# Performance work log

Hardware: AMD Instinct MI355X
Metric: run time of the kernel (lower is better)

The kernel has to match this reference:

```python
import jax, jax.numpy as jnp
import numpy as np

B, Q, D = 8, 1, 4096
NH, NKV, HD = 32, 8, 128
KV = 4096
ROPE_BASE = 10000.0


def setup_inputs() -> dict:
    key = jax.random.key(0)
    ks = jax.random.split(key, 10)
    s = 0.02  # realistic init scale for weights
    return {
        "hidden_states": jax.random.normal(ks[0], (B, Q, D), jnp.float32),
        "past_k": jax.random.normal(ks[1], (B, NH, KV, HD), jnp.float32),
        "past_v": jax.random.normal(ks[2], (B, NH, KV, HD), jnp.float32),
        "Wq": jax.random.normal(ks[3], (NH * HD, D), jnp.float32) * s,
        "bq": jax.random.normal(ks[4], (NH * HD,), jnp.float32) * s,
        "Wk": jax.random.normal(ks[5], (NKV * HD, D), jnp.float32) * s,
        "bk": jax.random.normal(ks[6], (NKV * HD,), jnp.float32) * s,
        "Wv": jax.random.normal(ks[7], (NKV * HD, D), jnp.float32) * s,
        "bv": jax.random.normal(ks[8], (NKV * HD,), jnp.float32) * s,
        "Wo": jax.random.normal(ks[9], (D, NH * HD), jnp.float32) * s,
        "position_ids": KV,  # current decode position (past length)
    }


def _rope(x, pos0):
    # x: [B, H, Q, HD]; rotate_half-style RoPE at positions pos0..pos0+Q-1
    half = HD // 2
    inv_freq = 1.0 / (ROPE_BASE ** (jnp.arange(half, dtype=jnp.float32) / half))
    pos = (pos0 + jnp.arange(Q)).astype(jnp.float32)          # [Q]
    ang = pos[:, None] * inv_freq[None, :]                    # [Q, half]
    cos = jnp.concatenate([jnp.cos(ang), jnp.cos(ang)], -1)   # [Q, HD]
    sin = jnp.concatenate([jnp.sin(ang), jnp.sin(ang)], -1)
    x1, x2 = x[..., :half], x[..., half:]
    rot = jnp.concatenate([-x2, x1], axis=-1)
    return x * cos + rot * sin


def reference(hidden_states, past_k, past_v, Wq, bq, Wk, bk, Wv, bv, Wo, position_ids):
    # QKV projections (Qwen: biased q/k/v, unbiased o)
    q = hidden_states @ Wq.T + bq   # [B, Q, NH*HD]
    k = hidden_states @ Wk.T + bk   # [B, Q, NKV*HD]
    v = hidden_states @ Wv.T + bv
    q = q.reshape(B, Q, NH, HD).transpose(0, 2, 1, 3)    # [B, NH, Q, HD]
    k = k.reshape(B, Q, NKV, HD).transpose(0, 2, 1, 3)   # [B, NKV, Q, HD]
    v = v.reshape(B, Q, NKV, HD).transpose(0, 2, 1, 3)
    # RoPE on current tokens only (past cache already rotated)
    q = _rope(q, position_ids)
    k = _rope(k, position_ids)
    # GQA repeat_interleave to full head count
    rep = NH // NKV
    k = jnp.repeat(k, rep, axis=1)   # [B, NH, Q, HD]
    v = jnp.repeat(v, rep, axis=1)
    # Assemble streaming KV window: past cache is stored post-repeat
    k = jnp.concatenate([past_k, k], axis=2)   # [B, NH, KV+Q, HD]
    v = jnp.concatenate([past_v, v], axis=2)
    scale = jnp.float32(1.0 / np.sqrt(HD))
    scores = jnp.einsum("bhqd,bhkd->bhqk", q, k) * scale   # [B, NH, Q, KV+Q]
    # causal: query positions KV..KV+Q-1 attend to key positions <= own pos
    qpos = KV + jnp.arange(Q)
    kpos = jnp.arange(KV + Q)
    mask = qpos[:, None] >= kpos[None, :]
    scores = jnp.where(mask, scores, jnp.float32(-1e30))
    attn = jax.nn.softmax(scores, axis=-1)
    ctx = jnp.einsum("bhqk,bhkd->bhqd", attn, v)           # [B, NH, Q, HD]
    ctx = ctx.transpose(0, 2, 1, 3).reshape(B, Q, NH * HD)
    return ctx @ Wo.T   # [B, Q, D]
```

## Files before the change

kernel.cpp:

```cpp
#include <hip/hip_runtime.h>
#include <hip/hip_bf16.h>
#include <math.h>

#define BB 8
#define DD 4096
#define NHQ 32
#define NKV 8
#define HD 128
#define KVL 4096
#define NSPLIT 32
#define CHUNK (KVL / NSPLIT)
#define SCALE 0.08838834764831845f

#define OFF_QROPE 0
#define OFF_KROPE (OFF_QROPE + BB*NHQ*HD)
#define OFF_VRAW  (OFF_KROPE + BB*NKV*HD)
#define OFF_PART  (OFF_VRAW  + BB*NKV*HD)
#define PART_STRIDE 132
#define OFF_CTX   (OFF_PART + BB*NHQ*NSPLIT*PART_STRIDE)

typedef float f32x4 __attribute__((ext_vector_type(4)));

__device__ __forceinline__ float4 ntload4(const float4* p) {
    f32x4 v = __builtin_nontemporal_load((const f32x4*)p);
    return make_float4(v.x, v.y, v.z, v.w);
}

__global__ __launch_bounds__(256) void k_qkv(
    const float* __restrict__ hs,
    const float* __restrict__ Wq, const float* __restrict__ bq,
    const float* __restrict__ Wk, const float* __restrict__ bk,
    const float* __restrict__ Wv, const float* __restrict__ bv,
    const int* __restrict__ posp,
    float* __restrict__ ws)
{
    const int wid  = threadIdx.x >> 6;
    const int lane = threadIdx.x & 63;
    const int w    = blockIdx.x * 4 + wid;

    const float* W; const float* bias; float* dst; int dstride; int r1; int i; bool rope;
    if (w < 2048) {
        const int h = w >> 6; i = w & 63; r1 = h*HD + i;
        W = Wq; bias = bq; dst = ws + OFF_QROPE; dstride = NHQ*HD; rope = true;
    } else if (w < 2560) {
        const int w2 = w - 2048; const int h = w2 >> 6; i = w2 & 63; r1 = h*HD + i;
        W = Wk; bias = bk; dst = ws + OFF_KROPE; dstride = NKV*HD; rope = true;
    } else {
        const int w3 = w - 2560; const int h = w3 >> 6; i = w3 & 63; r1 = h*HD + i;
        W = Wv; bias = bv; dst = ws + OFF_VRAW; dstride = NKV*HD; rope = false;
    }
    const int r2 = r1 + 64;

    const double pos = (double)posp[0];
    const double ang = pos * pow(10000.0, -(double)i / 64.0);
    const float c = (float)cos(ang), s = (float)sin(ang);

    const float4* WrA = (const float4*)(W + (size_t)r1 * DD);
    const float4* WrB = (const float4*)(W + (size_t)r2 * DD);
    const float4* H   = (const float4*)hs;

    float accA[BB], accB[BB];
    #pragma unroll
    for (int b = 0; b < BB; ++b) { accA[b] = 0.f; accB[b] = 0.f; }

    for (int it = 0; it < DD/256; ++it) {
        const int idx = it*64 + lane;
        const float4 wa = ntload4(&WrA[idx]);
        const float4 wb = ntload4(&WrB[idx]);
        #pragma unroll
        for (int b = 0; b < BB; ++b) {
            const float4 h4 = H[b*(DD/4) + idx];
            accA[b] = fmaf(wa.x, h4.x, fmaf(wa.y, h4.y, fmaf(wa.z, h4.z, fmaf(wa.w, h4.w, accA[b]))));
            accB[b] = fmaf(wb.x, h4.x, fmaf(wb.y, h4.y, fmaf(wb.z, h4.z, fmaf(wb.w, h4.w, accB[b]))));
        }
    }
    #pragma unroll
    for (int b = 0; b < BB; ++b) {
        float va = accA[b], vb = accB[b];
        #pragma unroll
        for (int off = 32; off; off >>= 1) {
            va += __shfl_xor(va, off, 64);
            vb += __shfl_xor(vb, off, 64);
        }
        accA[b] = va; accB[b] = vb;
    }
    if (lane == 0) {
        const float b1 = bias[r1], b2 = bias[r2];
        #pragma unroll
        for (int b = 0; b < BB; ++b) {
            const float a1 = accA[b] + b1;
            const float a2 = accB[b] + b2;
            float o1, o2;
            if (rope) { o1 = fmaf(a1, c, -a2*s); o2 = fmaf(a2, c, a1*s); }
            else      { o1 = a1;                 o2 = a2; }
            dst[(size_t)b*dstride + r1] = o1;
            dst[(size_t)b*dstride + r2] = o2;
        }
    }
}

__global__ __launch_bounds__(256) void k_attn(
    const float* __restrict__ Kc, const float* __restrict__ Vc,
    float* __restrict__ ws)
{
    const int wid  = threadIdx.x >> 6;
    const int lane = threadIdx.x & 63;
    const int sub  = lane >> 5, l32 = lane & 31;
    const int task  = blockIdx.x * 4 + wid;
    const int pair  = task >> 5;
    const int split = task & (NSPLIT - 1);
    const int b = pair >> 5, h = pair & 31;

    const float4 q4 = ((const float4*)(ws + OFF_QROPE + (size_t)pair * HD))[l32];
    const size_t base = ((size_t)pair * KVL + (size_t)split * CHUNK) * HD;
    const float4* Kp = (const float4*)(Kc + base);
    const float4* Vp = (const float4*)(Vc + base);

    float m = -1e30f, l = 0.f;
    float4 acc = {0.f, 0.f, 0.f, 0.f};

    for (int it = 0; it < CHUNK/8; ++it) {
        const int r0 = it*8 + sub;
        const float4 k0 = ntload4(&Kp[(r0+0)*32 + l32]);
        const float4 k1 = ntload4(&Kp[(r0+2)*32 + l32]);
        const float4 k2 = ntload4(&Kp[(r0+4)*32 + l32]);
        const float4 k3 = ntload4(&Kp[(r0+6)*32 + l32]);
        const float4 v0 = ntload4(&Vp[(r0+0)*32 + l32]);
        const float4 v1 = ntload4(&Vp[(r0+2)*32 + l32]);
        const float4 v2 = ntload4(&Vp[(r0+4)*32 + l32]);
        const float4 v3 = ntload4(&Vp[(r0+6)*32 + l32]);

        float s0 = fmaf(q4.x, k0.x, fmaf(q4.y, k0.y, fmaf(q4.z, k0.z, q4.w*k0.w)));
        float s1 = fmaf(q4.x, k1.x, fmaf(q4.y, k1.y, fmaf(q4.z, k1.z, q4.w*k1.w)));
        float s2 = fmaf(q4.x, k2.x, fmaf(q4.y, k2.y, fmaf(q4.z, k2.z, q4.w*k2.w)));
        float s3 = fmaf(q4.x, k3.x, fmaf(q4.y, k3.y, fmaf(q4.z, k3.z, q4.w*k3.w)));
        #pragma unroll
        for (int off = 16; off; off >>= 1) {
            s0 += __shfl_xor(s0, off, 64);
            s1 += __shfl_xor(s1, off, 64);
            s2 += __shfl_xor(s2, off, 64);
            s3 += __shfl_xor(s3, off, 64);
        }
        s0 *= SCALE; s1 *= SCALE; s2 *= SCALE; s3 *= SCALE;

        const float newm = fmaxf(fmaxf(fmaxf(s0, s1), fmaxf(s2, s3)), m);
        const float r_ = __expf(m - newm);
        const float e0 = __expf(s0 - newm);
        const float e1 = __expf(s1 - newm);
        const float e2 = __expf(s2 - newm);
        const float e3 = __expf(s3 - newm);
        m = newm;
        l = fmaf(l, r_, (e0 + e1) + (e2 + e3));
        acc.x = fmaf(acc.x, r_, fmaf(e0, v0.x, e1*v1.x) + fmaf(e2, v2.x, e3*v3.x));
        acc.y = fmaf(acc.y, r_, fmaf(e0, v0.y, e1*v1.y) + fmaf(e2, v2.y, e3*v3.y));
        acc.z = fmaf(acc.z, r_, fmaf(e0, v0.z, e1*v1.z) + fmaf(e2, v2.z, e3*v3.z));
        acc.w = fmaf(acc.w, r_, fmaf(e0, v0.w, e1*v1.w) + fmaf(e2, v2.w, e3*v3.w));
    }

    if (split == NSPLIT - 1 && sub == 0) {
        const float4 k4 = ((const float4*)(ws + OFF_KROPE + (size_t)(b*NKV + (h>>2)) * HD))[l32];
        const float4 v4 = ((const float4*)(ws + OFF_VRAW  + (size_t)(b*NKV + (h>>2)) * HD))[l32];
        float sv = fmaf(q4.x, k4.x, fmaf(q4.y, k4.y, fmaf(q4.z, k4.z, q4.w*k4.w)));
        #pragma unroll
        for (int off = 16; off; off >>= 1) sv += __shfl_xor(sv, off, 64);
        sv *= SCALE;
        const float newm = fmaxf(m, sv);
        const float r_ = __expf(m - newm);
        const float e  = __expf(sv - newm);
        m = newm;
        l = fmaf(l, r_, e);
        acc.x = fmaf(acc.x, r_, e*v4.x);
        acc.y = fmaf(acc.y, r_, e*v4.y);
        acc.z = fmaf(acc.z, r_, e*v4.z);
        acc.w = fmaf(acc.w, r_, e*v4.w);
    }

    const float M  = fmaxf(m, __shfl_xor(m, 32, 64));
    const float r_ = __expf(m - M);
    l *= r_; acc.x *= r_; acc.y *= r_; acc.z *= r_; acc.w *= r_;
    l     += __shfl_xor(l,     32, 64);
    acc.x += __shfl_xor(acc.x, 32, 64);
    acc.y += __shfl_xor(acc.y, 32, 64);
    acc.z += __shfl_xor(acc.z, 32, 64);
    acc.w += __shfl_xor(acc.w, 32, 64);

    if (sub == 0) {
        float* pp = ws + OFF_PART + ((size_t)pair * NSPLIT + split) * PART_STRIDE;
        ((float4*)pp)[l32] = acc;
        if (l32 == 0) { pp[HD] = M; pp[HD+1] = l; }
    }
}

__global__ __launch_bounds__(128) void k_combine(float* __restrict__ ws)
{
    const int pair = blockIdx.x;
    const int d = threadIdx.x;
    const float* pp = ws + OFF_PART + (size_t)pair * NSPLIT * PART_STRIDE;
    __shared__ float sm[NSPLIT], sl[NSPLIT];
    if (d < NSPLIT) { sm[d] = pp[d*PART_STRIDE + HD]; sl[d] = pp[d*PART_STRIDE + HD + 1]; }
    __syncthreads();
    float M = -1e30f;
    #pragma unroll
    for (int s = 0; s < NSPLIT; ++s) M = fmaxf(M, sm[s]);
    float L = 0.f, acc = 0.f;
    #pragma unroll 8
    for (int s = 0; s < NSPLIT; ++s) {
        const float w = expf(sm[s] - M);
        L += sl[s] * w;
        acc = fmaf(pp[s*PART_STRIDE + d], w, acc);
    }
    ws[OFF_CTX + (size_t)pair*HD + d] = acc / L;
}

__global__ __launch_bounds__(256) void k_oproj(
    const float* __restrict__ Wo, const float* __restrict__ ws, float* __restrict__ out)
{
    const int wid  = threadIdx.x >> 6;
    const int lane = threadIdx.x & 63;
    const int row  = blockIdx.x * 4 + wid;
    const float4* Wr = (const float4*)(Wo + (size_t)row * DD);
    const float4* C  = (const float4*)(ws + OFF_CTX);
    float acc[BB];
    #pragma unroll
    for (int b = 0; b < BB; ++b) acc[b] = 0.f;
    for (int it = 0; it < DD/256; ++it) {
        const int idx = it*64 + lane;
        const float4 w4 = ntload4(&Wr[idx]);
        #pragma unroll
        for (int b = 0; b < BB; ++b) {
            const float4 h4 = C[b*(DD/4) + idx];
            acc[b] = fmaf(w4.x, h4.x, fmaf(w4.y, h4.y, fmaf(w4.z, h4.z, fmaf(w4.w, h4.w, acc[b]))));
        }
    }
    #pragma unroll
    for (int b = 0; b < BB; ++b) {
        float v = acc[b];
        #pragma unroll
        for (int off = 32; off; off >>= 1) v += __shfl_xor(v, off, 64);
        if (lane == 0) out[(size_t)b*DD + row] = v;
    }
}

extern "C" void kernel_launch(void* const* d_in, const int* in_sizes, int n_in,
                              void* d_out, int out_size, void* d_ws, size_t ws_size,
                              hipStream_t stream)
{
    const float* hs  = (const float*)d_in[0];
    const float* pk  = (const float*)d_in[1];
    const float* pv  = (const float*)d_in[2];
    const float* Wq  = (const float*)d_in[3];
    const float* bq  = (const float*)d_in[4];
    const float* Wk  = (const float*)d_in[5];
    const float* bk  = (const float*)d_in[6];
    const float* Wv  = (const float*)d_in[7];
    const float* bv  = (const float*)d_in[8];
    const float* Wo  = (const float*)d_in[9];
    const int*   pos = (const int*)d_in[10];
    float* out = (float*)d_out;
    float* ws  = (float*)d_ws;

    k_qkv    <<<3072/4,          256, 0, stream>>>(hs, Wq, bq, Wk, bk, Wv, bv, pos, ws);
    k_attn   <<<BB*NHQ*NSPLIT/4, 256, 0, stream>>>(pk, pv, ws);
    k_combine<<<BB*NHQ,          128, 0, stream>>>(ws);
    k_oproj  <<<4096/4,          256, 0, stream>>>(Wo, ws, out);
}
```

Baseline: 248.0 us.

## Split attention chunk into two-pass scores-then-values with LDS-staged scores

Replaces the per-step online softmax in the attention kernel with two passes over each chunk. The first pass computes all QK scores, tracks the running max and stores the scores in shared memory. The second pass streams V and accumulates exp-weighted values against that fixed max, which removes the per-step rescaling exps and multiplies. In exchange, K and V are no longer loaded in the same loop, so less memory traffic is in flight per iteration in this bandwidth-bound kernel, and there are extra LDS writes and reads plus a 2 KB shared allocation per block.

```diff
diff --git a/kernel.cpp b/kernel.cpp
--- a/kernel.cpp
+++ b/kernel.cpp
@@ -24,6 +24,10 @@
 __device__ __forceinline__ float4 ntload4(const float4* p) {
     f32x4 v = __builtin_nontemporal_load((const f32x4*)p);
     return make_float4(v.x, v.y, v.z, v.w);
+}
+
+__device__ __forceinline__ float dot4(const float4 a, const float4 b) {
+    return fmaf(a.x, b.x, fmaf(a.y, b.y, fmaf(a.z, b.z, a.w*b.w)));
 }
 
 __global__ __launch_bounds__(256) void k_qkv(
@@ -103,6 +107,8 @@
     const float* __restrict__ Kc, const float* __restrict__ Vc,
     float* __restrict__ ws)
 {
+    __shared__ float sc_lds[4][CHUNK];
+
     const int wid  = threadIdx.x >> 6;
     const int lane = threadIdx.x & 63;
     const int sub  = lane >> 5, l32 = lane & 31;
@@ -110,30 +116,22 @@
     const int pair  = task >> 5;
     const int split = task & (NSPLIT - 1);
     const int b = pair >> 5, h = pair & 31;
+    float* swv = sc_lds[wid];
 
     const float4 q4 = ((const float4*)(ws + OFF_QROPE + (size_t)pair * HD))[l32];
     const size_t base = ((size_t)pair * KVL + (size_t)split * CHUNK) * HD;
     const float4* Kp = (const float4*)(Kc + base);
     const float4* Vp = (const float4*)(Vc + base);
 
-    float m = -1e30f, l = 0.f;
-    float4 acc = {0.f, 0.f, 0.f, 0.f};
-
+    float m0 = -1e30f;
     for (int it = 0; it < CHUNK/8; ++it) {
         const int r0 = it*8 + sub;
         const float4 k0 = ntload4(&Kp[(r0+0)*32 + l32]);
         const float4 k1 = ntload4(&Kp[(r0+2)*32 + l32]);
         const float4 k2 = ntload4(&Kp[(r0+4)*32 + l32]);
         const float4 k3 = ntload4(&Kp[(r0+6)*32 + l32]);
-        const float4 v0 = ntload4(&Vp[(r0+0)*32 + l32]);
-        const float4 v1 = ntload4(&Vp[(r0+2)*32 + l32]);
-        const float4 v2 = ntload4(&Vp[(r0+4)*32 + l32]);
-        const float4 v3 = ntload4(&Vp[(r0+6)*32 + l32]);
-
-        float s0 = fmaf(q4.x, k0.x, fmaf(q4.y, k0.y, fmaf(q4.z, k0.z, q4.w*k0.w)));
-        float s1 = fmaf(q4.x, k1.x, fmaf(q4.y, k1.y, fmaf(q4.z, k1.z, q4.w*k1.w)));
-        float s2 = fmaf(q4.x, k2.x, fmaf(q4.y, k2.y, fmaf(q4.z, k2.z, q4.w*k2.w)));
-        float s3 = fmaf(q4.x, k3.x, fmaf(q4.y, k3.y, fmaf(q4.z, k3.z, q4.w*k3.w)));
+        float s0 = dot4(q4, k0), s1 = dot4(q4, k1);
+        float s2 = dot4(q4, k2), s3 = dot4(q4, k3);
         #pragma unroll
         for (int off = 16; off; off >>= 1) {
             s0 += __shfl_xor(s0, off, 64);
@@ -142,25 +140,36 @@
             s3 += __shfl_xor(s3, off, 64);
         }
         s0 *= SCALE; s1 *= SCALE; s2 *= SCALE; s3 *= SCALE;
-
-        const float newm = fmaxf(fmaxf(fmaxf(s0, s1), fmaxf(s2, s3)), m);
-        const float r_ = __expf(m - newm);
-        const float e0 = __expf(s0 - newm);
-        const float e1 = __expf(s1 - newm);
-        const float e2 = __expf(s2 - newm);
-        const float e3 = __expf(s3 - newm);
-        m = newm;
-        l = fmaf(l, r_, (e0 + e1) + (e2 + e3));
-        acc.x = fmaf(acc.x, r_, fmaf(e0, v0.x, e1*v1.x) + fmaf(e2, v2.x, e3*v3.x));
-        acc.y = fmaf(acc.y, r_, fmaf(e0, v0.y, e1*v1.y) + fmaf(e2, v2.y, e3*v3.y));
-        acc.z = fmaf(acc.z, r_, fmaf(e0, v0.z, e1*v1.z) + fmaf(e2, v2.z, e3*v3.z));
-        acc.w = fmaf(acc.w, r_, fmaf(e0, v0.w, e1*v1.w) + fmaf(e2, v2.w, e3*v3.w));
+        m0 = fmaxf(m0, fmaxf(fmaxf(s0, s1), fmaxf(s2, s3)));
+        if (l32 == 0) {
+            swv[r0+0] = s0; swv[r0+2] = s1; swv[r0+4] = s2; swv[r0+6] = s3;
+        }
+    }
+    float m = fmaxf(m0, __shfl_xor(m0, 32, 64));
+
+    float l = 0.f;
+    float4 acc = {0.f, 0.f, 0.f, 0.f};
+    for (int it = 0; it < CHUNK/8; ++it) {
+        const int r0 = it*8 + sub;
+        const float4 v0 = ntload4(&Vp[(r0+0)*32 + l32]);
+        const float4 v1 = ntload4(&Vp[(r0+2)*32 + l32]);
+        const float4 v2 = ntload4(&Vp[(r0+4)*32 + l32]);
+        const float4 v3 = ntload4(&Vp[(r0+6)*32 + l32]);
+        const float e0 = __expf(swv[r0+0] - m);
+        const float e1 = __expf(swv[r0+2] - m);
+        const float e2 = __expf(swv[r0+4] - m);
+        const float e3 = __expf(swv[r0+6] - m);
+        l += (e0 + e1) + (e2 + e3);
+        acc.x += fmaf(e0, v0.x, e1*v1.x) + fmaf(e2, v2.x, e3*v3.x);
+        acc.y += fmaf(e0, v0.y, e1*v1.y) + fmaf(e2, v2.y, e3*v3.y);
+        acc.z += fmaf(e0, v0.z, e1*v1.z) + fmaf(e2, v2.z, e3*v3.z);
+        acc.w += fmaf(e0, v0.w, e1*v1.w) + fmaf(e2, v2.w, e3*v3.w);
     }
 
     if (split == NSPLIT - 1 && sub == 0) {
-        const float4 k4 = ((const float4*)(ws + OFF_KROPE + (size_t)(b*NKV + (h>>2)) * HD))[l32];
-        const float4 v4 = ((const float4*)(ws + OFF_VRAW  + (size_t)(b*NKV + (h>>2)) * HD))[l32];
-        float sv = fmaf(q4.x, k4.x, fmaf(q4.y, k4.y, fmaf(q4.z, k4.z, q4.w*k4.w)));
+        const float4 kn = ((const float4*)(ws + OFF_KROPE + (size_t)(b*NKV + (h>>2)) * HD))[l32];
+        const float4 vn = ((const float4*)(ws + OFF_VRAW  + (size_t)(b*NKV + (h>>2)) * HD))[l32];
+        float sv = dot4(q4, kn);
         #pragma unroll
         for (int off = 16; off; off >>= 1) sv += __shfl_xor(sv, off, 64);
         sv *= SCALE;
@@ -169,15 +178,15 @@
         const float e  = __expf(sv - newm);
         m = newm;
         l = fmaf(l, r_, e);
-        acc.x = fmaf(acc.x, r_, e*v4.x);
-        acc.y = fmaf(acc.y, r_, e*v4.y);
-        acc.z = fmaf(acc.z, r_, e*v4.z);
-        acc.w = fmaf(acc.w, r_, e*v4.w);
+        acc.x = fmaf(acc.x, r_, e*vn.x);
+        acc.y = fmaf(acc.y, r_, e*vn.y);
+        acc.z = fmaf(acc.z, r_, e*vn.z);
+        acc.w = fmaf(acc.w, r_, e*vn.w);
     }
 
     const float M  = fmaxf(m, __shfl_xor(m, 32, 64));
-    const float r_ = __expf(m - M);
-    l *= r_; acc.x *= r_; acc.y *= r_; acc.z *= r_; acc.w *= r_;
+    const float r2_ = __expf(m - M);
+    l *= r2_; acc.x *= r2_; acc.y *= r2_; acc.z *= r2_; acc.w *= r2_;
     l     += __shfl_xor(l,     32, 64);
     acc.x += __shfl_xor(acc.x, 32, 64);
     acc.y += __shfl_xor(acc.y, 32, 64);
```

Result: no change. 246.0 us (median of 3 runs) (-0.8%).
